# Kernel tuning notes

Hardware: AMD Instinct MI355X
Metric: run time of the kernel (lower is better)

The kernel has to match this reference:

```python
import jax, jax.numpy as jnp
import numpy as np

# Model hyperparameters (match init_kwargs)
NUM_HEADS = 12
KEY_SIZE = 64
VALUE_SIZE = 64
D_MODEL = 768
NUM_LAYERS = 4
FFW = 3072
B, T, L = 2, 32, 256
LN_EPS = 1e-5


def _layer_norm(x, scale, offset):
    m = jnp.mean(x, axis=-1, keepdims=True)
    v = jnp.mean(jnp.square(x - m), axis=-1, keepdims=True)
    return (x - m) * jax.lax.rsqrt(v + LN_EPS) * scale + offset


def _axial_attn(x, Wq, Wk, Wv, Wo, bo, mode):
    # x: [B, T, L, D]
    b, t, l, d = x.shape
    q = (x @ Wq).reshape(b, t, l, NUM_HEADS, KEY_SIZE)
    k = (x @ Wk).reshape(b, t, l, NUM_HEADS, KEY_SIZE)
    v = (x @ Wv).reshape(b, t, l, NUM_HEADS, VALUE_SIZE)
    inv_sqrt_d = KEY_SIZE ** (-0.5)
    if mode == 'time':
        logits = jnp.einsum('btlhd,bTlhd->blhtT', q, k) * inv_sqrt_d
        w = jax.nn.softmax(logits, axis=-1)
        a = jnp.einsum('blhtT,bTlhd->btlhd', w, v)
    else:  # space
        logits = jnp.einsum('btlhd,btLhd->bthlL', q, k) * inv_sqrt_d
        w = jax.nn.softmax(logits, axis=-1)
        a = jnp.einsum('bthlL,btLhd->btlhd', w, v)
    a = a.reshape(b, t, l, NUM_HEADS * VALUE_SIZE)
    return a @ Wo + bo


def _forward(input_embeddings, Wq_t, Wk_t, Wv_t, Wo_t, bo_t,
             Wq_s, Wk_s, Wv_s, Wo_s, bo_s,
             ln_t_scale, ln_t_bias, ln_s_scale, ln_s_bias,
             ln2_scale, ln2_bias, W1, b1, W2, b2):
    def block(h, p):
        (wq_t, wk_t, wv_t, wo_t, bot, wq_s, wk_s, wv_s, wo_s, bos,
         lts, ltb, lss, lsb, l2s, l2b, w1, bb1, w2, bb2) = p
        # time attention + residual
        x = _layer_norm(h, lts, ltb)
        h = h + _axial_attn(x, wq_t, wk_t, wv_t, wo_t, bot, 'time')
        # space attention + residual
        x = _layer_norm(h, lss, lsb)
        h = h + _axial_attn(x, wq_s, wk_s, wv_s, wo_s, bos, 'space')
        # FFN + residual
        x = _layer_norm(h, l2s, l2b)
        ff = jax.nn.gelu(x @ w1 + bb1) @ w2 + bb2
        return h + ff, None

    params = (Wq_t, Wk_t, Wv_t, Wo_t, bo_t, Wq_s, Wk_s, Wv_s, Wo_s, bo_s,
              ln_t_scale, ln_t_bias, ln_s_scale, ln_s_bias,
              ln2_scale, ln2_bias, W1, b1, W2, b2)
    h, _ = jax.lax.scan(block, input_embeddings, params)
    return h


def setup_inputs() -> dict:
    key = jax.random.key(0)
    ks = jax.random.split(key, 32)
    D, H, KD, VD, F, NL = D_MODEL, NUM_HEADS, KEY_SIZE, VALUE_SIZE, FFW, NUM_LAYERS
    init_scale = 2.0 / np.sqrt(NL)  # VarianceScaling scale used by the module
    s_in = np.sqrt(init_scale / D).astype(np.float32)   # fan_in = D
    s_out = np.sqrt(init_scale / (H * VD)).astype(np.float32)
    s_ffw2 = np.sqrt(init_scale / F).astype(np.float32)
    x = jax.random.normal(ks[0], (B, T, L, D), dtype=jnp.float32)
    def nrm(k, shape, s):
        return jax.random.normal(k, shape, dtype=jnp.float32) * s
    inp = {
        'input_embeddings': x,
        'Wq_t': nrm(ks[1], (NL, D, H * KD), s_in),
        'Wk_t': nrm(ks[2], (NL, D, H * KD), s_in),
        'Wv_t': nrm(ks[3], (NL, D, H * VD), s_in),
        'Wo_t': nrm(ks[4], (NL, H * VD, D), s_out),
        'bo_t': jnp.zeros((NL, D), jnp.float32),
        'Wq_s': nrm(ks[5], (NL, D, H * KD), s_in),
        'Wk_s': nrm(ks[6], (NL, D, H * KD), s_in),
        'Wv_s': nrm(ks[7], (NL, D, H * VD), s_in),
        'Wo_s': nrm(ks[8], (NL, H * VD, D), s_out),
        'bo_s': jnp.zeros((NL, D), jnp.float32),
        'ln_t_scale': jnp.ones((NL, D), jnp.float32),
        'ln_t_bias': jnp.zeros((NL, D), jnp.float32),
        'ln_s_scale': jnp.ones((NL, D), jnp.float32),
        'ln_s_bias': jnp.zeros((NL, D), jnp.float32),
        'ln2_scale': jnp.ones((NL, D), jnp.float32),
        'ln2_bias': jnp.zeros((NL, D), jnp.float32),
        'W1': nrm(ks[9], (NL, D, F), s_in),
        'b1': jnp.zeros((NL, F), jnp.float32),
        'W2': nrm(ks[10], (NL, F, D), s_ffw2),
        'b2': jnp.zeros((NL, D), jnp.float32),
    }
    return inp


def reference(input_embeddings, Wq_t, Wk_t, Wv_t, Wo_t, bo_t,
              Wq_s, Wk_s, Wv_s, Wo_s, bo_s,
              ln_t_scale, ln_t_bias, ln_s_scale, ln_s_bias,
              ln2_scale, ln2_bias, W1, b1, W2, b2):
    return _forward(input_embeddings, Wq_t, Wk_t, Wv_t, Wo_t, bo_t,
                    Wq_s, Wk_s, Wv_s, Wo_s, bo_s,
                    ln_t_scale, ln_t_bias, ln_s_scale, ln_s_bias,
                    ln2_scale, ln2_bias, W1, b1, W2, b2)
```

## Files before the change

kernel.cpp:

```cpp
#include <hip/hip_runtime.h>


#define AS1 __attribute__((address_space(1)))
#define AS3 __attribute__((address_space(3)))

using bf16x8 = __attribute__((ext_vector_type(8))) short;
using f32x4  = __attribute__((ext_vector_type(4))) float;

__device__ __forceinline__ f32x4 mfma_bf16(bf16x8 a, bf16x8 b, f32x4 c) {
  return __builtin_amdgcn_mfma_f32_16x16x32_bf16(a, b, c, 0, 0, 0);
}

__device__ __forceinline__ void async16(const void* g, void* l) {
  __builtin_amdgcn_global_load_lds((const AS1 void*)g, (AS3 void*)l, 16, 0, 0);
}

__device__ __forceinline__ short f2bs(float f) {
  union { float f; unsigned u; } x; x.f = f;
  unsigned r = x.u + 0x7fffu + ((x.u >> 16) & 1u);
  return (short)(r >> 16);
}

__device__ __forceinline__ f32x4 fzero() {
  f32x4 v; v[0] = 0.f; v[1] = 0.f; v[2] = 0.f; v[3] = 0.f; return v;
}

__device__ __forceinline__ float quad16_max(float v) {
  v = fmaxf(v, __shfl_xor(v, 1));
  v = fmaxf(v, __shfl_xor(v, 2));
  v = fmaxf(v, __shfl_xor(v, 4));
  v = fmaxf(v, __shfl_xor(v, 8));
  return v;
}
__device__ __forceinline__ float quad16_sum(float v) {
  v += __shfl_xor(v, 1); v += __shfl_xor(v, 2);
  v += __shfl_xor(v, 4); v += __shfl_xor(v, 8);
  return v;
}

template<int MODE>
__global__ __launch_bounds__(512, 2) void gemm256(
    const short* __restrict__ A, const short* __restrict__ BT,
    const float* __restrict__ bias, const float* __restrict__ resid,
    float* __restrict__ outF, short* __restrict__ outB,
    int M, int N, int K, int nx)
{
  __shared__ __align__(16) short lds[65536];
  (void)M;
  const int tid  = threadIdx.x;
  const int wave = tid >> 6, lane = tid & 63;
  const int quad = lane >> 4, l16 = lane & 15;
  const int wm = wave >> 2, wn = wave & 3;

  const unsigned flat = blockIdx.x;
  const unsigned su = flat >> 3;
  const unsigned nxu = (unsigned)nx;
  const long bm0 = (long)((flat & 7u) + 8u * (su / nxu)) * 256;
  const long bn0 = (long)(su % nxu) * 256;

  const int srow = lane >> 2;
  const int skof = ((lane & 3) ^ ((lane >> 3) & 3)) * 8;
  const int r0 = wave * 32;
  const short* gA0 = A  + (bm0 + r0 + srow) * (long)K + skof;
  const short* gA1 = gA0 + 16 * (long)K;
  const short* gB0 = BT + (bn0 + r0 + srow) * (long)K + skof;
  const short* gB1 = gB0 + 16 * (long)K;
  char* const lbase = (char*)lds;
  const int dA0 = r0 * 64, dA1 = (r0 + 16) * 64;
  const int dB0 = 16384 + r0 * 64, dB1 = 16384 + (r0 + 16) * 64;

  int aoff[8], boff[4];
#pragma unroll
  for (int i = 0; i < 8; ++i) {
    int row = wm * 128 + i * 16 + l16;
    aoff[i] = row * 32 + (quad ^ ((row >> 1) & 3)) * 8;
  }
#pragma unroll
  for (int j = 0; j < 4; ++j) {
    int row = wn * 64 + j * 16 + l16;
    boff[j] = 8192 + row * 32 + (quad ^ ((row >> 1) & 3)) * 8;
  }

  f32x4 acc[8][4];
#pragma unroll
  for (int i = 0; i < 8; ++i)
#pragma unroll
    for (int j = 0; j < 4; ++j) acc[i][j] = fzero();

  const int nt = K >> 5;

#define STAGE(t)                                                         \
  do {                                                                   \
    const int sb_ = ((t) & 3) * 32768;                                   \
    const long ko_ = (long)(t) * 32;                                     \
    async16(gA0 + ko_, lbase + sb_ + dA0);                               \
    async16(gA1 + ko_, lbase + sb_ + dA1);                               \
    async16(gB0 + ko_, lbase + sb_ + dB0);                               \
    async16(gB1 + ko_, lbase + sb_ + dB1);                               \
  } while (0)

  STAGE(0); STAGE(1); STAGE(2);

  for (int t = 0; t < nt; ++t) {
    if (t + 3 < nt) STAGE(t + 3);
    const int ahead = nt - 1 - t;
    if (ahead >= 3)      asm volatile("s_waitcnt vmcnt(12)" ::: "memory");
    else if (ahead == 2) asm volatile("s_waitcnt vmcnt(8)"  ::: "memory");
    else if (ahead == 1) asm volatile("s_waitcnt vmcnt(4)"  ::: "memory");
    else                 asm volatile("s_waitcnt vmcnt(0)"  ::: "memory");
    __builtin_amdgcn_s_barrier();
    asm volatile("" ::: "memory");
    __builtin_amdgcn_sched_barrier(0);

    const short* sbase = lds + (t & 3) * 16384;
    bf16x8 a[8], b[4];
#pragma unroll
    for (int i = 0; i < 8; ++i) a[i] = *(const bf16x8*)(sbase + aoff[i]);
#pragma unroll
    for (int j = 0; j < 4; ++j) b[j] = *(const bf16x8*)(sbase + boff[j]);
    asm volatile("s_waitcnt lgkmcnt(0)" ::: "memory");
    __builtin_amdgcn_sched_barrier(0);
    __builtin_amdgcn_s_barrier();

    __builtin_amdgcn_s_setprio(1);
#pragma unroll
    for (int i = 0; i < 8; ++i)
#pragma unroll
      for (int j = 0; j < 4; ++j)
        acc[i][j] = mfma_bf16(a[i], b[j], acc[i][j]);
    __builtin_amdgcn_s_setprio(0);
  }
#undef STAGE

  const long rowbase = bm0 + wm * 128 + quad * 4;
  const long colbase = bn0 + wn * 64 + l16;
#pragma unroll
  for (int i = 0; i < 8; ++i)
#pragma unroll
    for (int j = 0; j < 4; ++j) {
      const long gc = colbase + j * 16;
#pragma unroll
      for (int r = 0; r < 4; ++r) {
        const long gr = rowbase + i * 16 + r;
        const size_t idx = (size_t)gr * N + gc;
        float v = acc[i][j][r];
        if (MODE == 0) {
          outB[idx] = f2bs(v);
        } else if (MODE == 1) {
          outF[idx] = v + bias[gc] + resid[idx];
        } else {
          float tt = v + bias[gc];
          float g = 0.5f * tt * (1.f + tanhf(0.7978845608f * (tt + 0.044715f * tt * tt * tt)));
          outB[idx] = f2bs(g);
        }
      }
    }
}

__global__ __launch_bounds__(256) void ln_kernel(
    const float* __restrict__ h, const float* __restrict__ sc,
    const float* __restrict__ bi, short* __restrict__ out)
{
  const int row = blockIdx.x, tid = threadIdx.x;
  const float* hr = h + (long)row * 768;
  float x0 = hr[tid], x1 = hr[tid + 256], x2 = hr[tid + 512];
  __shared__ float red[4];
  float s = x0 + x1 + x2;
#pragma unroll
  for (int m = 32; m >= 1; m >>= 1) s += __shfl_xor(s, m);
  if ((tid & 63) == 0) red[tid >> 6] = s;
  __syncthreads();
  float mean = (red[0] + red[1] + red[2] + red[3]) * (1.f / 768.f);
  float d0 = x0 - mean, d1 = x1 - mean, d2 = x2 - mean;
  float q = d0 * d0 + d1 * d1 + d2 * d2;
#pragma unroll
  for (int m = 32; m >= 1; m >>= 1) q += __shfl_xor(q, m);
  __syncthreads();
  if ((tid & 63) == 0) red[tid >> 6] = q;
  __syncthreads();
  float var = (red[0] + red[1] + red[2] + red[3]) * (1.f / 768.f);
  float inv = rsqrtf(var + 1e-5f);
  long o = (long)row * 768;
  out[o + tid]       = f2bs(d0 * inv * sc[tid]       + bi[tid]);
  out[o + tid + 256] = f2bs(d1 * inv * sc[tid + 256] + bi[tid + 256]);
  out[o + tid + 512] = f2bs(d2 * inv * sc[tid + 512] + bi[tid + 512]);
}

__global__ __launch_bounds__(256) void transpose_w(
    const float* __restrict__ in, short* __restrict__ out, int Kd, int Nd,
    long inStride, long outStride)
{
  __shared__ float t[32][33];
  const int z = blockIdx.z;
  in  += (long)z * inStride;
  out += (long)z * outStride;
  const int n0 = blockIdx.x * 32, k0 = blockIdx.y * 32;
  const int r = threadIdx.x >> 5, c = threadIdx.x & 31;
#pragma unroll
  for (int rr = 0; rr < 4; ++rr)
    t[r + rr * 8][c] = in[(long)(k0 + r + rr * 8) * Nd + n0 + c];
  __syncthreads();
#pragma unroll
  for (int rr = 0; rr < 4; ++rr)
    out[(long)(n0 + r + rr * 8) * Kd + k0 + c] = f2bs(t[c][r + rr * 8]);
}

__global__ __launch_bounds__(256) void attn_space(
    const short* __restrict__ qkv, short* __restrict__ ao)
{
  __shared__ __align__(16) short VT[64 * 256];
  __shared__ __align__(16) short P[4][16 * 256];
  const int qt = blockIdx.x, hh = blockIdx.y, bt = blockIdx.z;
  const long tok0 = (long)bt * 256;
  const int tid = threadIdx.x, wave = tid >> 6, lane = tid & 63;
  const int quad = lane >> 4, l16 = lane & 15;

#pragma unroll
  for (int it = 0; it < 8; ++it) {
    int chunk = it * 256 + tid;
    int vl = chunk >> 3, d8 = (chunk & 7) * 8;
    bf16x8 v = *(const bf16x8*)(qkv + (tok0 + vl) * 2304 + 1536 + hh * 64 + d8);
#pragma unroll
    for (int e = 0; e < 8; ++e) VT[(d8 + e) * 256 + vl] = v[e];
  }

  const int qr = qt * 64 + wave * 16;
  bf16x8 qf[2];
#pragma unroll
  for (int kk = 0; kk < 2; ++kk)
    qf[kk] = *(const bf16x8*)(qkv + (tok0 + qr + l16) * 2304 + hh * 64 + kk * 32 + quad * 8);

  f32x4 S[16];
#pragma unroll
  for (int j = 0; j < 16; ++j) S[j] = fzero();
#pragma unroll
  for (int j = 0; j < 16; ++j)
#pragma unroll
    for (int kk = 0; kk < 2; ++kk) {
      bf16x8 kf = *(const bf16x8*)(qkv + (tok0 + j * 16 + l16) * 2304 + 768 + hh * 64 + kk * 32 + quad * 8);
      S[j] = mfma_bf16(qf[kk], kf, S[j]);
    }

#pragma unroll
  for (int r = 0; r < 4; ++r) {
    float m = -1e30f;
#pragma unroll
    for (int j = 0; j < 16; ++j) m = fmaxf(m, S[j][r]);
    m = quad16_max(m);
    float sum = 0.f;
#pragma unroll
    for (int j = 0; j < 16; ++j) {
      float e = __expf((S[j][r] - m) * 0.125f);
      S[j][r] = e; sum += e;
    }
    sum = quad16_sum(sum);
    float inv = 1.f / sum;
#pragma unroll
    for (int j = 0; j < 16; ++j)
      P[wave][(quad * 4 + r) * 256 + j * 16 + l16] = f2bs(S[j][r] * inv);
  }
  __syncthreads();

  f32x4 O[4];
#pragma unroll
  for (int jn = 0; jn < 4; ++jn) O[jn] = fzero();
  for (int kk = 0; kk < 8; ++kk) {
    bf16x8 pf = *(const bf16x8*)&P[wave][l16 * 256 + kk * 32 + quad * 8];
#pragma unroll
    for (int jn = 0; jn < 4; ++jn) {
      bf16x8 vf = *(const bf16x8*)&VT[(jn * 16 + l16) * 256 + kk * 32 + quad * 8];
      O[jn] = mfma_bf16(pf, vf, O[jn]);
    }
  }
#pragma unroll
  for (int jn = 0; jn < 4; ++jn)
#pragma unroll
    for (int r = 0; r < 4; ++r) {
      int row = qr + quad * 4 + r;
      ao[(tok0 + row) * 768 + hh * 64 + jn * 16 + l16] = f2bs(O[jn][r]);
    }
}

__global__ __launch_bounds__(64) void attn_time(
    const short* __restrict__ qkv, short* __restrict__ ao)
{
  __shared__ __align__(16) short VT[64 * 32];
  __shared__ __align__(16) short P[32 * 32];
  const int ll = blockIdx.x, hh = blockIdx.y, b = blockIdx.z;
  const int lane = threadIdx.x;
  const int quad = lane >> 4, l16 = lane & 15;
#define TOK(t) (((long)(b * 32 + (t))) * 256 + ll)

#pragma unroll
  for (int it = 0; it < 4; ++it) {
    int chunk = it * 64 + lane;
    int t = chunk >> 3, d8 = (chunk & 7) * 8;
    bf16x8 v = *(const bf16x8*)(qkv + TOK(t) * 2304 + 1536 + hh * 64 + d8);
#pragma unroll
    for (int e = 0; e < 8; ++e) VT[(d8 + e) * 32 + t] = v[e];
  }

  bf16x8 qf[2][2];
#pragma unroll
  for (int mi = 0; mi < 2; ++mi)
#pragma unroll
    for (int kk = 0; kk < 2; ++kk)
      qf[mi][kk] = *(const bf16x8*)(qkv + TOK(mi * 16 + l16) * 2304 + hh * 64 + kk * 32 + quad * 8);

  f32x4 S[2][2];
#pragma unroll
  for (int mi = 0; mi < 2; ++mi) { S[mi][0] = fzero(); S[mi][1] = fzero(); }
#pragma unroll
  for (int nj = 0; nj < 2; ++nj)
#pragma unroll
    for (int kk = 0; kk < 2; ++kk) {
      bf16x8 kf = *(const bf16x8*)(qkv + TOK(nj * 16 + l16) * 2304 + 768 + hh * 64 + kk * 32 + quad * 8);
#pragma unroll
      for (int mi = 0; mi < 2; ++mi)
        S[mi][nj] = mfma_bf16(qf[mi][kk], kf, S[mi][nj]);
    }

#pragma unroll
  for (int mi = 0; mi < 2; ++mi)
#pragma unroll
    for (int r = 0; r < 4; ++r) {
      float m = fmaxf(S[mi][0][r], S[mi][1][r]);
      m = quad16_max(m);
      float e0 = __expf((S[mi][0][r] - m) * 0.125f);
      float e1 = __expf((S[mi][1][r] - m) * 0.125f);
      float sum = quad16_sum(e0 + e1);
      float inv = 1.f / sum;
      P[(mi * 16 + quad * 4 + r) * 32 + l16]      = f2bs(e0 * inv);
      P[(mi * 16 + quad * 4 + r) * 32 + 16 + l16] = f2bs(e1 * inv);
    }
  __syncthreads();

  f32x4 O[2][4];
#pragma unroll
  for (int mi = 0; mi < 2; ++mi)
#pragma unroll
    for (int jn = 0; jn < 4; ++jn) O[mi][jn] = fzero();
#pragma unroll
  for (int mi = 0; mi < 2; ++mi) {
    bf16x8 pf = *(const bf16x8*)&P[(mi * 16 + l16) * 32 + quad * 8];
#pragma unroll
    for (int jn = 0; jn < 4; ++jn) {
      bf16x8 vf = *(const bf16x8*)&VT[(jn * 16 + l16) * 32 + quad * 8];
      O[mi][jn] = mfma_bf16(pf, vf, O[mi][jn]);
    }
  }
#pragma unroll
  for (int mi = 0; mi < 2; ++mi)
#pragma unroll
    for (int jn = 0; jn < 4; ++jn)
#pragma unroll
      for (int r = 0; r < 4; ++r) {
        int t = mi * 16 + quad * 4 + r;
        ao[TOK(t) * 768 + hh * 64 + jn * 16 + l16] = f2bs(O[mi][jn][r]);
      }
#undef TOK
}

extern "C" void kernel_launch(void* const* d_in, const int* in_sizes, int n_in,
                              void* d_out, int out_size, void* d_ws, size_t ws_size,
                              hipStream_t stream)
{
  const float* emb     = (const float*)d_in[0];
  const float* Wq_t    = (const float*)d_in[1];
  const float* Wk_t    = (const float*)d_in[2];
  const float* Wv_t    = (const float*)d_in[3];
  const float* Wo_t    = (const float*)d_in[4];
  const float* bo_t    = (const float*)d_in[5];
  const float* Wq_s    = (const float*)d_in[6];
  const float* Wk_s    = (const float*)d_in[7];
  const float* Wv_s    = (const float*)d_in[8];
  const float* Wo_s    = (const float*)d_in[9];
  const float* bo_s    = (const float*)d_in[10];
  const float* ln_t_sc = (const float*)d_in[11];
  const float* ln_t_bi = (const float*)d_in[12];
  const float* ln_s_sc = (const float*)d_in[13];
  const float* ln_s_bi = (const float*)d_in[14];
  const float* ln2_sc  = (const float*)d_in[15];
  const float* ln2_bi  = (const float*)d_in[16];
  const float* W1      = (const float*)d_in[17];
  const float* b1      = (const float*)d_in[18];
  const float* W2      = (const float*)d_in[19];
  const float* b2      = (const float*)d_in[20];

  const long M = 16384, D = 768, QN = 2304, F = 3072;
  char* ws = (char*)d_ws;
  size_t off = 0;
  auto alloc = [&](size_t b) { char* p = ws + off; off += (b + 255) & ~(size_t)255; return p; };
  short* qkvT_t = (short*)alloc((size_t)4 * QN * D * 2);
  short* qkvT_s = (short*)alloc((size_t)4 * QN * D * 2);
  short* woT_t  = (short*)alloc((size_t)4 * D * D * 2);
  short* woT_s  = (short*)alloc((size_t)4 * D * D * 2);
  short* w1T    = (short*)alloc((size_t)4 * F * D * 2);
  short* w2T    = (short*)alloc((size_t)4 * D * F * 2);
  short* xb     = (short*)alloc((size_t)M * D * 2);
  short* aob    = (short*)alloc((size_t)M * D * 2);
  short* big    = (short*)alloc((size_t)M * F * 2);
  float* h = (float*)d_out;

  hipMemcpyAsync(h, emb, (size_t)M * D * 4, hipMemcpyDeviceToDevice, stream);

  transpose_w<<<dim3(24, 24, 4), 256, 0, stream>>>(Wq_t, qkvT_t,             768, 768,  D * D, QN * D);
  transpose_w<<<dim3(24, 24, 4), 256, 0, stream>>>(Wk_t, qkvT_t + D * D,     768, 768,  D * D, QN * D);
  transpose_w<<<dim3(24, 24, 4), 256, 0, stream>>>(Wv_t, qkvT_t + 2 * D * D, 768, 768,  D * D, QN * D);
  transpose_w<<<dim3(24, 24, 4), 256, 0, stream>>>(Wq_s, qkvT_s,             768, 768,  D * D, QN * D);
  transpose_w<<<dim3(24, 24, 4), 256, 0, stream>>>(Wk_s, qkvT_s + D * D,     768, 768,  D * D, QN * D);
  transpose_w<<<dim3(24, 24, 4), 256, 0, stream>>>(Wv_s, qkvT_s + 2 * D * D, 768, 768,  D * D, QN * D);
  transpose_w<<<dim3(24, 24, 4), 256, 0, stream>>>(Wo_t, woT_t,              768, 768,  D * D, D * D);
  transpose_w<<<dim3(24, 24, 4), 256, 0, stream>>>(Wo_s, woT_s,              768, 768,  D * D, D * D);
  transpose_w<<<dim3(96, 24, 4), 256, 0, stream>>>(W1,   w1T,                768, 3072, D * F, F * D);
  transpose_w<<<dim3(24, 96, 4), 256, 0, stream>>>(W2,   w2T,                3072, 768, F * D, D * F);

  for (int l = 0; l < 4; ++l) {
    ln_kernel<<<16384, 256, 0, stream>>>(h, ln_t_sc + l * 768, ln_t_bi + l * 768, xb);
    gemm256<0><<<9 * 64, 512, 0, stream>>>(xb, qkvT_t + (long)l * QN * D,
        nullptr, nullptr, nullptr, big, 16384, 2304, 768, 9);
    attn_time<<<dim3(256, 12, 2), 64, 0, stream>>>(big, aob);
    gemm256<1><<<3 * 64, 512, 0, stream>>>(aob, woT_t + (long)l * D * D,
        bo_t + l * 768, h, h, nullptr, 16384, 768, 768, 3);
    ln_kernel<<<16384, 256, 0, stream>>>(h, ln_s_sc + l * 768, ln_s_bi + l * 768, xb);
    gemm256<0><<<9 * 64, 512, 0, stream>>>(xb, qkvT_s + (long)l * QN * D,
        nullptr, nullptr, nullptr, big, 16384, 2304, 768, 9);
    attn_space<<<dim3(4, 12, 64), 256, 0, stream>>>(big, aob);
    gemm256<1><<<3 * 64, 512, 0, stream>>>(aob, woT_s + (long)l * D * D,
        bo_s + l * 768, h, h, nullptr, 16384, 768, 768, 3);
    ln_kernel<<<16384, 256, 0, stream>>>(h, ln2_sc + l * 768, ln2_bi + l * 768, xb);
    gemm256<2><<<12 * 64, 512, 0, stream>>>(xb, w1T + (long)l * F * D,
        b1 + l * 3072, nullptr, nullptr, big, 16384, 3072, 768, 12);
    gemm256<1><<<3 * 64, 512, 0, stream>>>(big, w2T + (long)l * D * F,
        b2 + l * 768, h, h, nullptr, 16384, 768, 3072, 3);
  }
}
```

Measured before the change: 2.733 ms.

## Restructure GEMM mainloop into BK=64 double-buffered ping-pong quadrant schedule

```diff
diff --git a/kernel.cpp b/kernel.cpp
--- a/kernel.cpp
+++ b/kernel.cpp
@@ -48,7 +48,7 @@
   __shared__ __align__(16) short lds[65536];
   (void)M;
   const int tid  = threadIdx.x;
-  const int wave = tid >> 6, lane = tid & 63;
+  const int lane = tid & 63, wave = tid >> 6;
   const int quad = lane >> 4, l16 = lane & 15;
   const int wm = wave >> 2, wn = wave & 3;
 
@@ -58,28 +58,22 @@
   const long bm0 = (long)((flat & 7u) + 8u * (su / nxu)) * 256;
   const long bn0 = (long)(su % nxu) * 256;
 
-  const int srow = lane >> 2;
-  const int skof = ((lane & 3) ^ ((lane >> 3) & 3)) * 8;
-  const int r0 = wave * 32;
-  const short* gA0 = A  + (bm0 + r0 + srow) * (long)K + skof;
-  const short* gA1 = gA0 + 16 * (long)K;
-  const short* gB0 = BT + (bn0 + r0 + srow) * (long)K + skof;
-  const short* gB1 = gB0 + 16 * (long)K;
-  char* const lbase = (char*)lds;
-  const int dA0 = r0 * 64, dA1 = (r0 + 16) * 64;
-  const int dB0 = 16384 + r0 * 64, dB1 = 16384 + (r0 + 16) * 64;
-
-  int aoff[8], boff[4];
-#pragma unroll
-  for (int i = 0; i < 8; ++i) {
-    int row = wm * 128 + i * 16 + l16;
-    aoff[i] = row * 32 + (quad ^ ((row >> 1) & 3)) * 8;
-  }
-#pragma unroll
-  for (int j = 0; j < 4; ++j) {
-    int row = wn * 64 + j * 16 + l16;
-    boff[j] = 8192 + row * 32 + (quad ^ ((row >> 1) & 3)) * 8;
-  }
+  const int trow = tid >> 3;
+  const int tg   = ((tid & 7) ^ (trow & 7)) * 8;
+  const short* As = A  + (bm0 + trow) * (long)K + tg;
+  const short* Bs = BT + (bn0 + trow) * (long)K + tg;
+
+  auto STAGE = [&](int tile, int isB, int half) {
+    const short* sp = (isB ? Bs : As) + (long)half * 128 * K + (long)tile * 64;
+    char* db = (char*)lds + (tile & 1) * 65536 + isB * 32768 + half * 16384
+             + (tid << 4);
+    async16(sp, db);
+    async16(sp + ((long)K << 6), db + 8192);
+  };
+
+  const int swg   = (quad ^ (l16 & 7)) * 8;
+  const int arow0 = wm * 128 + l16;
+  const int brow0 = wn * 64 + l16;
 
   f32x4 acc[8][4];
 #pragma unroll
@@ -87,50 +81,101 @@
 #pragma unroll
     for (int j = 0; j < 4; ++j) acc[i][j] = fzero();
 
-  const int nt = K >> 5;
-
-#define STAGE(t)                                                         \
-  do {                                                                   \
-    const int sb_ = ((t) & 3) * 32768;                                   \
-    const long ko_ = (long)(t) * 32;                                     \
-    async16(gA0 + ko_, lbase + sb_ + dA0);                               \
-    async16(gA1 + ko_, lbase + sb_ + dA1);                               \
-    async16(gB0 + ko_, lbase + sb_ + dB0);                               \
-    async16(gB1 + ko_, lbase + sb_ + dB1);                               \
-  } while (0)
-
-  STAGE(0); STAGE(1); STAGE(2);
-
-  for (int t = 0; t < nt; ++t) {
-    if (t + 3 < nt) STAGE(t + 3);
-    const int ahead = nt - 1 - t;
-    if (ahead >= 3)      asm volatile("s_waitcnt vmcnt(12)" ::: "memory");
-    else if (ahead == 2) asm volatile("s_waitcnt vmcnt(8)"  ::: "memory");
-    else if (ahead == 1) asm volatile("s_waitcnt vmcnt(4)"  ::: "memory");
-    else                 asm volatile("s_waitcnt vmcnt(0)"  ::: "memory");
-    __builtin_amdgcn_s_barrier();
-    asm volatile("" ::: "memory");
-    __builtin_amdgcn_sched_barrier(0);
-
-    const short* sbase = lds + (t & 3) * 16384;
-    bf16x8 a[8], b[4];
-#pragma unroll
-    for (int i = 0; i < 8; ++i) a[i] = *(const bf16x8*)(sbase + aoff[i]);
-#pragma unroll
-    for (int j = 0; j < 4; ++j) b[j] = *(const bf16x8*)(sbase + boff[j]);
+  const int nt = K >> 6;
+
+  STAGE(0, 0, 0); STAGE(0, 0, 1); STAGE(0, 1, 0); STAGE(0, 1, 1);
+  STAGE(1, 1, 0); STAGE(1, 1, 1);
+  asm volatile("s_waitcnt vmcnt(4)" ::: "memory");
+  __builtin_amdgcn_s_barrier();
+  __builtin_amdgcn_sched_barrier(0);
+
+  for (int u = 0; u < nt; ++u) {
+    const short* bufA = lds + (u & 1) * 32768;
+    const short* bufB = bufA + 16384;
+    bf16x8 a[4][2], b[4][2];
+
+#pragma unroll
+    for (int i = 0; i < 4; ++i) {
+      a[i][0] = *(const bf16x8*)(bufA + (arow0 + i * 16) * 64 + swg);
+      a[i][1] = *(const bf16x8*)(bufA + (arow0 + i * 16) * 64 + (swg ^ 32));
+    }
+#pragma unroll
+    for (int j = 0; j < 2; ++j) {
+      b[j][0] = *(const bf16x8*)(bufB + (brow0 + j * 16) * 64 + swg);
+      b[j][1] = *(const bf16x8*)(bufB + (brow0 + j * 16) * 64 + (swg ^ 32));
+    }
+    if (u + 1 < nt) STAGE(u + 1, 0, 0);
+    asm volatile("s_waitcnt lgkmcnt(8)" ::: "memory");
+    __builtin_amdgcn_s_barrier();
     asm volatile("s_waitcnt lgkmcnt(0)" ::: "memory");
     __builtin_amdgcn_sched_barrier(0);
-    __builtin_amdgcn_s_barrier();
-
     __builtin_amdgcn_s_setprio(1);
 #pragma unroll
-    for (int i = 0; i < 8; ++i)
-#pragma unroll
-      for (int j = 0; j < 4; ++j)
-        acc[i][j] = mfma_bf16(a[i], b[j], acc[i][j]);
+    for (int kk = 0; kk < 2; ++kk)
+#pragma unroll
+      for (int i = 0; i < 4; ++i)
+#pragma unroll
+        for (int j = 0; j < 2; ++j)
+          acc[i][j] = mfma_bf16(a[i][kk], b[j][kk], acc[i][j]);
     __builtin_amdgcn_s_setprio(0);
-  }
-#undef STAGE
+    __builtin_amdgcn_s_barrier();
+
+#pragma unroll
+    for (int j = 2; j < 4; ++j) {
+      b[j][0] = *(const bf16x8*)(bufB + (brow0 + j * 16) * 64 + swg);
+      b[j][1] = *(const bf16x8*)(bufB + (brow0 + j * 16) * 64 + (swg ^ 32));
+    }
+    if (u + 1 < nt) STAGE(u + 1, 0, 1);
+    __builtin_amdgcn_s_barrier();
+    asm volatile("s_waitcnt lgkmcnt(0)" ::: "memory");
+    __builtin_amdgcn_sched_barrier(0);
+    __builtin_amdgcn_s_setprio(1);
+#pragma unroll
+    for (int kk = 0; kk < 2; ++kk)
+#pragma unroll
+      for (int i = 0; i < 4; ++i)
+#pragma unroll
+        for (int j = 2; j < 4; ++j)
+          acc[i][j] = mfma_bf16(a[i][kk], b[j][kk], acc[i][j]);
+    __builtin_amdgcn_s_setprio(0);
+    __builtin_amdgcn_s_barrier();
+
+#pragma unroll
+    for (int i = 0; i < 4; ++i) {
+      a[i][0] = *(const bf16x8*)(bufA + (arow0 + 64 + i * 16) * 64 + swg);
+      a[i][1] = *(const bf16x8*)(bufA + (arow0 + 64 + i * 16) * 64 + (swg ^ 32));
+    }
+    if (u + 2 < nt) STAGE(u + 2, 1, 0);
+    __builtin_amdgcn_s_barrier();
+    asm volatile("s_waitcnt lgkmcnt(0)" ::: "memory");
+    __builtin_amdgcn_sched_barrier(0);
+    __builtin_amdgcn_s_setprio(1);
+#pragma unroll
+    for (int kk = 0; kk < 2; ++kk)
+#pragma unroll
+      for (int i = 0; i < 4; ++i)
+#pragma unroll
+        for (int j = 2; j < 4; ++j)
+          acc[4 + i][j] = mfma_bf16(a[i][kk], b[j][kk], acc[4 + i][j]);
+    __builtin_amdgcn_s_setprio(0);
+    __builtin_amdgcn_s_barrier();
+
+    if (u + 2 < nt) STAGE(u + 2, 1, 1);
+    __builtin_amdgcn_s_barrier();
+    __builtin_amdgcn_s_setprio(1);
+#pragma unroll
+    for (int kk = 0; kk < 2; ++kk)
+#pragma unroll
+      for (int i = 0; i < 4; ++i)
+#pragma unroll
+        for (int j = 0; j < 2; ++j)
+          acc[4 + i][j] = mfma_bf16(a[i][kk], b[j][kk], acc[4 + i][j]);
+    __builtin_amdgcn_s_setprio(0);
+    if (u + 2 < nt) asm volatile("s_waitcnt vmcnt(4)" ::: "memory");
+    else            asm volatile("s_waitcnt vmcnt(0)" ::: "memory");
+    __builtin_amdgcn_s_barrier();
+    __builtin_amdgcn_sched_barrier(0);
+  }
 
   const long rowbase = bm0 + wm * 128 + quad * 4;
   const long colbase = bn0 + wn * 64 + l16;
@@ -150,7 +195,8 @@
           outF[idx] = v + bias[gc] + resid[idx];
         } else {
           float tt = v + bias[gc];
-          float g = 0.5f * tt * (1.f + tanhf(0.7978845608f * (tt + 0.044715f * tt * tt * tt)));
+          float z = 0.7978845608f * (tt + 0.044715f * tt * tt * tt);
+          float g = __fdividef(tt, 1.f + __expf(-2.f * z));
           outB[idx] = f2bs(g);
         }
       }
```

Result: faster. 2.554 ms (-6.6%).
